# Kernel optimization log

Hardware: AMD Instinct MI355X
Metric: run time of the kernel (lower is better)

Reference implementation:

```python
import jax, jax.numpy as jnp
import numpy as np

N_NODES = 100000
N_EDGES = 1600000
IN_CH, HID_CH, LAT = 32, 32, 16


def _gcn_layer(h, W, b, src, dst, norm):
    # PyG GCNConv: h' = scatter_add(norm * (h W)[src] -> dst) + b
    h = h @ W                                   # [N, out]
    msg = h[src] * norm[:, None]                # [E+N, out] gather
    out = jax.ops.segment_sum(msg, dst, num_segments=N_NODES)
    return out + b


def setup_inputs() -> dict:
    key = jax.random.key(0)
    ks = jax.random.split(key, 8)
    x = jax.random.normal(ks[0], (N_NODES, IN_CH), dtype=jnp.float32)
    edge_index = jax.random.randint(ks[1], (2, N_EDGES), 0, N_NODES, dtype=jnp.int32)
    def glorot(k, fan_in, fan_out):
        lim = np.sqrt(6.0 / (fan_in + fan_out)).astype(np.float32)
        return jax.random.uniform(k, (fan_in, fan_out), jnp.float32, -lim, lim)
    return {
        "x": x,
        "edge_index": edge_index,
        "W1": glorot(ks[2], IN_CH, HID_CH),
        "b1": jnp.zeros((HID_CH,), jnp.float32),
        "Wmu": glorot(ks[3], HID_CH, LAT),
        "bmu": jnp.zeros((LAT,), jnp.float32),
        "Wlv": glorot(ks[4], HID_CH, LAT),
        "blv": jnp.zeros((LAT,), jnp.float32),
    }


def reference(x, edge_index, W1, b1, Wmu, bmu, Wlv, blv):
    # Add self-loops (GCNConv default add_self_loops=True)
    loops = jnp.arange(N_NODES, dtype=edge_index.dtype)
    src = jnp.concatenate([edge_index[0], loops])
    dst = jnp.concatenate([edge_index[1], loops])
    # Symmetric normalization: deg over destinations, norm = d^-1/2[src] * d^-1/2[dst]
    deg = jax.ops.segment_sum(jnp.ones_like(dst, dtype=x.dtype), dst,
                              num_segments=N_NODES)
    dinv = jnp.where(deg > 0, jax.lax.rsqrt(deg), 0.0)
    norm = dinv[src] * dinv[dst]                # [E+N]

    h = jax.nn.relu(_gcn_layer(x, W1, b1, src, dst, norm))
    mu = _gcn_layer(h, Wmu, bmu, src, dst, norm)
    logvar = _gcn_layer(h, Wlv, blv, src, dst, norm)
    return (mu, logvar)
```

## Files before the change

### kernel.cpp

```cpp
#include <hip/hip_runtime.h>
#include <hip/hip_fp16.h>

#define N_NODES 100000
#define N_EDGES 1600000
#define NCB 782
#define CAPC 2560
#define P1_BLOCKS 391
#define BKN 128
#define NBF_G 1563


__global__ __launch_bounds__(1024) void k_part1(const int* __restrict__ src,
                                                const int* __restrict__ dst,
                                                int* __restrict__ cursor1,
                                                unsigned* __restrict__ packed1) {
    __shared__ int bh[NCB];
    __shared__ int base[NCB];
    int t = threadIdx.x;
    for (int i = t; i < NCB; i += 1024) bh[i] = 0;
    __syncthreads();
    int g = blockIdx.x * 1024 + t;
    int d[4], s[4], r[4];
    if (g < N_EDGES / 4) {
        int4 d4 = reinterpret_cast<const int4*>(dst)[g];
        int4 s4 = reinterpret_cast<const int4*>(src)[g];
        d[0] = d4.x; d[1] = d4.y; d[2] = d4.z; d[3] = d4.w;
        s[0] = s4.x; s[1] = s4.y; s[2] = s4.z; s[3] = s4.w;
    } else {
        d[0] = d[1] = d[2] = d[3] = -1;
    }
#pragma unroll
    for (int j = 0; j < 4; ++j)
        if (d[j] >= 0) r[j] = atomicAdd(&bh[((unsigned)d[j]) >> 7], 1);
    __syncthreads();
    for (int i = t; i < NCB; i += 1024) {
        int c = bh[i];
        base[i] = i * CAPC + ((c > 0) ? atomicAdd(&cursor1[i], c) : 0);
    }
    __syncthreads();
#pragma unroll
    for (int j = 0; j < 4; ++j) {
        if (d[j] < 0) continue;
        unsigned dd = (unsigned)d[j];
        int b = dd >> 7;
        int pos = base[b] + r[j];
        if (pos < (b + 1) * CAPC)
            packed1[pos] = ((dd & 127u) << 17) | (unsigned)s[j];
    }
}

__global__ __launch_bounds__(512) void k_csrx(const unsigned* __restrict__ packed1,
                                              const int* __restrict__ cursor1,
                                              const float* __restrict__ x,
                                              const float* __restrict__ W1,
                                              unsigned* __restrict__ rowPack,
                                              int* __restrict__ srcSorted,
                                              __half* __restrict__ p1) {
    __shared__ int cnt[BKN];
    __shared__ int stt[BKN];
    __shared__ int wtot;
    __shared__ float sW[1024];
    int t = threadIdx.x;
    int b = blockIdx.x;
    int seg0 = b * CAPC;
    int cc = cursor1[b]; if (cc > CAPC) cc = CAPC;
    int segEnd = seg0 + cc;
    if (t < BKN) cnt[t] = 0;
    for (int i = t; i < 1024; i += 512) sW[i] = W1[i];
    unsigned pk[5]; int rk[5];
    {
        uint4 q = reinterpret_cast<const uint4*>(packed1 + seg0)[t];
        int i0 = seg0 + 4 * t;
        pk[0] = (i0     < segEnd) ? q.x : 0xFFFFFFFFu;
        pk[1] = (i0 + 1 < segEnd) ? q.y : 0xFFFFFFFFu;
        pk[2] = (i0 + 2 < segEnd) ? q.z : 0xFFFFFFFFu;
        pk[3] = (i0 + 3 < segEnd) ? q.w : 0xFFFFFFFFu;
        int i4 = seg0 + 2048 + t;
        pk[4] = (i4 < segEnd) ? packed1[i4] : 0xFFFFFFFFu;
    }
    float xv[8];
    int lane = t & 31;
    int rbase = t >> 5;
#pragma unroll
    for (int q = 0; q < 8; ++q) {
        int nd = b * BKN + rbase + q * 16;
        xv[q] = (nd < N_NODES) ? x[nd * 32 + lane] : 0.f;
    }
    __syncthreads();
#pragma unroll
    for (int j = 0; j < 5; ++j)
        if (pk[j] != 0xFFFFFFFFu) rk[j] = atomicAdd(&cnt[pk[j] >> 17], 1);
    __syncthreads();
    int v = 0, run = 0;
    if (t < BKN) {
        v = cnt[t];
        run = v;
#pragma unroll
        for (int off = 1; off < 64; off <<= 1) {
            int u = __shfl_up(run, off, 64);
            if ((t & 63) >= off) run += u;
        }
        if (t == 63) wtot = run;
    }
    __syncthreads();
    if (t < BKN) {
        if (t >= 64) run += wtot;
        int start = seg0 + run - v;
        stt[t] = start;
        int node = b * BKN + t;
        if (node < N_NODES) {
            int vc = (v < 2047) ? v : 2047;
            rowPack[node] = (unsigned)start | ((unsigned)vc << 21);
        }
    }
    __syncthreads();
#pragma unroll
    for (int j = 0; j < 5; ++j) {
        if (pk[j] == 0xFFFFFFFFu) continue;
        int pos = stt[pk[j] >> 17] + rk[j];
        srcSorted[pos] = (int)(pk[j] & 0x1FFFFu);
    }
#pragma unroll
    for (int q = 0; q < 8; ++q) {
        int r = rbase + q * 16;
        int nd = b * BKN + r;
        if (nd > N_NODES) break;
        if (nd == N_NODES) {
            p1[nd * 32 + lane] = __float2half(0.f);
            continue;
        }
        float a = 0.f;
#pragma unroll
        for (int k = 0; k < 32; ++k) {
            float xk = __shfl(xv[q], k, 32);
            a += xk * sW[k * 32 + lane];
        }
        float di = rsqrtf((float)(cnt[r] + 1));
        p1[nd * 32 + lane] = __float2half(di * a);
    }
}

__device__ __forceinline__ __half2 h2of(const float4& v, int c) {
    return reinterpret_cast<const __half2*>(&v)[c];
}

__device__ __forceinline__ void gatherRow4(const int* __restrict__ srcSorted,
                                           const float4* __restrict__ P,
                                           int beg, int end, int l,
                                           float* __restrict__ acc ) {
    for (int base = beg; base < end; base += 16) {
        int i0 = base + l,      i1 = base + 4 + l;
        int i2 = base + 8 + l,  i3 = base + 12 + l;
        int sA = (i0 < end) ? srcSorted[i0] : N_NODES;
        int sB = (i1 < end) ? srcSorted[i1] : N_NODES;
        int sC = (i2 < end) ? srcSorted[i2] : N_NODES;
        int sD = (i3 < end) ? srcSorted[i3] : N_NODES;
        float4 v0 = P[__shfl(sA, 0, 4) * 4 + l];
        float4 v1 = P[__shfl(sA, 1, 4) * 4 + l];
        float4 v2 = P[__shfl(sA, 2, 4) * 4 + l];
        float4 v3 = P[__shfl(sA, 3, 4) * 4 + l];
        float4 v4 = P[__shfl(sB, 0, 4) * 4 + l];
        float4 v5 = P[__shfl(sB, 1, 4) * 4 + l];
        float4 v6 = P[__shfl(sB, 2, 4) * 4 + l];
        float4 v7 = P[__shfl(sB, 3, 4) * 4 + l];
        float4 v8 = P[__shfl(sC, 0, 4) * 4 + l];
        float4 v9 = P[__shfl(sC, 1, 4) * 4 + l];
        float4 va = P[__shfl(sC, 2, 4) * 4 + l];
        float4 vb = P[__shfl(sC, 3, 4) * 4 + l];
        float4 vc = P[__shfl(sD, 0, 4) * 4 + l];
        float4 vd = P[__shfl(sD, 1, 4) * 4 + l];
        float4 ve = P[__shfl(sD, 2, 4) * 4 + l];
        float4 vf = P[__shfl(sD, 3, 4) * 4 + l];
#pragma unroll
        for (int c = 0; c < 4; ++c) {
            __half2 s01 = __hadd2(h2of(v0, c), h2of(v1, c));
            __half2 s23 = __hadd2(h2of(v2, c), h2of(v3, c));
            __half2 s45 = __hadd2(h2of(v4, c), h2of(v5, c));
            __half2 s67 = __hadd2(h2of(v6, c), h2of(v7, c));
            __half2 s89 = __hadd2(h2of(v8, c), h2of(v9, c));
            __half2 sab = __hadd2(h2of(va, c), h2of(vb, c));
            __half2 scd = __hadd2(h2of(vc, c), h2of(vd, c));
            __half2 sef = __hadd2(h2of(ve, c), h2of(vf, c));
            __half2 sum = __hadd2(__hadd2(__hadd2(s01, s23), __hadd2(s45, s67)),
                                  __hadd2(__hadd2(s89, sab), __hadd2(scd, sef)));
            float2 f = __half22float2(sum);
            acc[2 * c]     += f.x;
            acc[2 * c + 1] += f.y;
        }
    }
}

__global__ __launch_bounds__(256) void k_gx2(const unsigned* __restrict__ rowPack,
                                             const int* __restrict__ srcSorted,
                                             const __half* __restrict__ p1,
                                             const float* __restrict__ b1,
                                             const float* __restrict__ Wmu,
                                             const float* __restrict__ Wlv,
                                             __half* __restrict__ p2) {
    __shared__ float sW[1024];
    __shared__ float sB[32];
    int t = threadIdx.x;
    for (int i = t; i < 1024; i += 256) {
        int k = i >> 5, oc = i & 31;
        sW[i] = (oc < 16) ? Wmu[k * 16 + oc] : Wlv[k * 16 + (oc - 16)];
    }
    if (t < 32) sB[t] = b1[t];
    __syncthreads();
    int l = t & 3;
    int node = blockIdx.x * 64 + (t >> 2);
    if (node > N_NODES) return;
    const float4* P = (const float4*)p1;
    if (node == N_NODES) {
        ((float4*)p2)[node * 4 + l] = make_float4(0.f, 0.f, 0.f, 0.f);
        return;
    }
    unsigned rp = rowPack[node];
    int beg = (int)(rp & 0x1FFFFFu);
    int dg  = (int)(rp >> 21);
    float di = rsqrtf((float)(dg + 1));
    float acc[8] = {0.f, 0.f, 0.f, 0.f, 0.f, 0.f, 0.f, 0.f};
    gatherRow4(srcSorted, P, beg, beg + dg, l, acc);
    float4 ps = P[node * 4 + l];
    float h[8];
#pragma unroll
    for (int c = 0; c < 4; ++c) {
        float2 f = __half22float2(h2of(ps, c));
        h[2 * c]     = fmaxf(di * (acc[2 * c]     + f.x) + sB[8 * l + 2 * c],     0.f);
        h[2 * c + 1] = fmaxf(di * (acc[2 * c + 1] + f.y) + sB[8 * l + 2 * c + 1], 0.f);
    }
    float o[8] = {0.f, 0.f, 0.f, 0.f, 0.f, 0.f, 0.f, 0.f};
    const float4* W4 = (const float4*)sW;
#pragma unroll
    for (int m = 0; m < 4; ++m) {
#pragma unroll
        for (int j = 0; j < 8; ++j) {
            float hk = __shfl(h[j], m, 4);
            int k = 8 * m + j;
            float4 wa = W4[k * 8 + 2 * l];
            float4 wb = W4[k * 8 + 2 * l + 1];
            o[0] += hk * wa.x; o[1] += hk * wa.y; o[2] += hk * wa.z; o[3] += hk * wa.w;
            o[4] += hk * wb.x; o[5] += hk * wb.y; o[6] += hk * wb.z; o[7] += hk * wb.w;
        }
    }
    __half2 r0 = __floats2half2_rn(di * o[0], di * o[1]);
    __half2 r1 = __floats2half2_rn(di * o[2], di * o[3]);
    __half2 r2 = __floats2half2_rn(di * o[4], di * o[5]);
    __half2 r3 = __floats2half2_rn(di * o[6], di * o[7]);
    float4 st;
    st.x = *reinterpret_cast<float*>(&r0);
    st.y = *reinterpret_cast<float*>(&r1);
    st.z = *reinterpret_cast<float*>(&r2);
    st.w = *reinterpret_cast<float*>(&r3);
    ((float4*)p2)[node * 4 + l] = st;
}

__global__ __launch_bounds__(256) void k_gfin(const unsigned* __restrict__ rowPack,
                                              const int* __restrict__ srcSorted,
                                              const __half* __restrict__ p2,
                                              const float* __restrict__ bmu,
                                              const float* __restrict__ blv,
                                              float* __restrict__ out) {
    __shared__ float sB[32];
    int t = threadIdx.x;
    if (t < 32) sB[t] = (t < 16) ? bmu[t] : blv[t - 16];
    __syncthreads();
    int l = t & 3;
    int node = blockIdx.x * 64 + (t >> 2);
    if (node >= N_NODES) return;
    const float4* P = (const float4*)p2;
    unsigned rp = rowPack[node];
    int beg = (int)(rp & 0x1FFFFFu);
    int dg  = (int)(rp >> 21);
    float di = rsqrtf((float)(dg + 1));
    float acc[8] = {0.f, 0.f, 0.f, 0.f, 0.f, 0.f, 0.f, 0.f};
    gatherRow4(srcSorted, P, beg, beg + dg, l, acc);
    float4 ps = P[node * 4 + l];
    float v[8];
#pragma unroll
    for (int c = 0; c < 4; ++c) {
        float2 f = __half22float2(h2of(ps, c));
        v[2 * c]     = di * (acc[2 * c]     + f.x) + sB[8 * l + 2 * c];
        v[2 * c + 1] = di * (acc[2 * c + 1] + f.y) + sB[8 * l + 2 * c + 1];
    }
    float4 o0 = make_float4(v[0], v[1], v[2], v[3]);
    float4 o1 = make_float4(v[4], v[5], v[6], v[7]);
    float4* dst4 = (l < 2) ? (float4*)out
                           : (float4*)(out + (size_t)N_NODES * 16);
    int b4 = node * 4 + (l & 1) * 2;
    dst4[b4]     = o0;
    dst4[b4 + 1] = o1;
}

extern "C" void kernel_launch(void* const* d_in, const int* in_sizes, int n_in,
                              void* d_out, int out_size, void* d_ws, size_t ws_size,
                              hipStream_t stream) {
    const float* x   = (const float*)d_in[0];
    const int*   ei  = (const int*)d_in[1];
    const float* W1  = (const float*)d_in[2];
    const float* b1  = (const float*)d_in[3];
    const float* Wmu = (const float*)d_in[4];
    const float* bmu = (const float*)d_in[5];
    const float* Wlv = (const float*)d_in[6];
    const float* blv = (const float*)d_in[7];
    float* out = (float*)d_out;

    const int* src = ei;
    const int* dst = ei + N_EDGES;

    size_t off = 0;
    int* cursor1 = (int*)d_ws;                          off += NCB;
    unsigned* rowPack = (unsigned*)((int*)d_ws + off);  off += N_NODES;
    off = (off + 63) & ~(size_t)63;
    unsigned* packed1 = (unsigned*)((int*)d_ws + off);  off += (size_t)NCB * CAPC;
    off = (off + 63) & ~(size_t)63;
    int* srcSorted    = (int*)d_ws + off;               off += (size_t)NCB * CAPC;
    off = (off + 63) & ~(size_t)63;
    __half* p1h = (__half*)((int*)d_ws + off);          off += (size_t)(N_NODES + 1) * 16;
    off = (off + 63) & ~(size_t)63;
    __half* p2h = (__half*)((int*)d_ws + off);

    hipMemsetAsync(d_ws, 0, (size_t)NCB * sizeof(int), stream);
    k_part1<<<P1_BLOCKS, 1024, 0, stream>>>(src, dst, cursor1, packed1);
    k_csrx <<<NCB, 512, 0, stream>>>(packed1, cursor1, x, W1,
                                     rowPack, srcSorted, p1h);
    k_gx2  <<<NBF_G, 256, 0, stream>>>(rowPack, srcSorted, p1h,
                                       b1, Wmu, Wlv, p2h);
    k_gfin <<<NBF_G, 256, 0, stream>>>(rowPack, srcSorted, p2h,
                                       bmu, blv, out);
}
```

Before: 178.8 us.

## Group nodes by degree class within each bucket to balance gather work

The CSR build kernel now sorts the 128 nodes of each bucket into eight degree classes and writes a slot-indexed node id and packed row descriptor. The two gather kernels walk these slots instead of node ids, so nodes with similar degree share a wavefront and lane divergence in the edge loop drops. The padding row of p2 is zeroed in the CSR kernel, and the grid grows to cover all 782×128 slots. The cost is an extra indirection load per node and scattered, non-contiguous output writes.

Result: slower. 187.0 us (+4.6%).

```diff
diff --git a/kernel.cpp b/kernel.cpp
--- a/kernel.cpp
+++ b/kernel.cpp
@@ -7,7 +7,7 @@
 #define CAPC 2560
 #define P1_BLOCKS 391
 #define BKN 128
-#define NBF_G 1563
+#define NBF_G 1564
 
 
 __global__ __launch_bounds__(1024) void k_part1(const int* __restrict__ src,
@@ -53,12 +53,16 @@
                                               const int* __restrict__ cursor1,
                                               const float* __restrict__ x,
                                               const float* __restrict__ W1,
-                                              unsigned* __restrict__ rowPack,
+                                              int* __restrict__ nodeOf,
+                                              unsigned* __restrict__ rp2,
                                               int* __restrict__ srcSorted,
-                                              __half* __restrict__ p1) {
+                                              __half* __restrict__ p1,
+                                              __half* __restrict__ p2) {
     __shared__ int cnt[BKN];
     __shared__ int stt[BKN];
     __shared__ int wtot;
+    __shared__ int clsCnt[8];
+    __shared__ int clsOff[8];
     __shared__ float sW[1024];
     int t = threadIdx.x;
     int b = blockIdx.x;
@@ -66,7 +70,10 @@
     int cc = cursor1[b]; if (cc > CAPC) cc = CAPC;
     int segEnd = seg0 + cc;
     if (t < BKN) cnt[t] = 0;
+    if (t >= BKN && t < BKN + 8) clsCnt[t - BKN] = 0;
     for (int i = t; i < 1024; i += 512) sW[i] = W1[i];
+    if (b == 0 && t >= BKN + 8 && t < BKN + 12)
+        ((float4*)p2)[N_NODES * 4 + (t - BKN - 8)] = make_float4(0.f, 0.f, 0.f, 0.f);
     unsigned pk[5]; int rk[5];
     {
         uint4 q = reinterpret_cast<const uint4*>(packed1 + seg0)[t];
@@ -91,9 +98,11 @@
     for (int j = 0; j < 5; ++j)
         if (pk[j] != 0xFFFFFFFFu) rk[j] = atomicAdd(&cnt[pk[j] >> 17], 1);
     __syncthreads();
-    int v = 0, run = 0;
+    int v = 0, run = 0, myrank = 0, cls = 0;
     if (t < BKN) {
         v = cnt[t];
+        cls = (v + 15) >> 4; if (cls > 7) cls = 7;
+        myrank = atomicAdd(&clsCnt[cls], 1);
         run = v;
 #pragma unroll
         for (int off = 1; off < 64; off <<= 1) {
@@ -103,15 +112,14 @@
         if (t == 63) wtot = run;
     }
     __syncthreads();
+    if (t == 0) {
+        int s = 0;
+#pragma unroll
+        for (int c2 = 0; c2 < 8; ++c2) { clsOff[c2] = s; s += clsCnt[c2]; }
+    }
     if (t < BKN) {
         if (t >= 64) run += wtot;
-        int start = seg0 + run - v;
-        stt[t] = start;
-        int node = b * BKN + t;
-        if (node < N_NODES) {
-            int vc = (v < 2047) ? v : 2047;
-            rowPack[node] = (unsigned)start | ((unsigned)vc << 21);
-        }
+        stt[t] = seg0 + run - v;
     }
     __syncthreads();
 #pragma unroll
@@ -119,6 +127,13 @@
         if (pk[j] == 0xFFFFFFFFu) continue;
         int pos = stt[pk[j] >> 17] + rk[j];
         srcSorted[pos] = (int)(pk[j] & 0x1FFFFu);
+    }
+    if (t < BKN) {
+        int node = b * BKN + t;
+        int slot = b * BKN + clsOff[cls] + myrank;
+        int vc = (v < 2047) ? v : 2047;
+        nodeOf[slot] = (node < N_NODES) ? node : N_NODES;
+        rp2[slot] = (unsigned)stt[t] | ((unsigned)vc << 21);
     }
 #pragma unroll
     for (int q = 0; q < 8; ++q) {
@@ -190,7 +205,8 @@
     }
 }
 
-__global__ __launch_bounds__(256) void k_gx2(const unsigned* __restrict__ rowPack,
+__global__ __launch_bounds__(256) void k_gx2(const int* __restrict__ nodeOf,
+                                             const unsigned* __restrict__ rp2,
                                              const int* __restrict__ srcSorted,
                                              const __half* __restrict__ p1,
                                              const float* __restrict__ b1,
@@ -207,14 +223,11 @@
     if (t < 32) sB[t] = b1[t];
     __syncthreads();
     int l = t & 3;
-    int node = blockIdx.x * 64 + (t >> 2);
-    if (node > N_NODES) return;
+    int slot = blockIdx.x * 64 + (t >> 2);
+    int node = nodeOf[slot];
+    if (node >= N_NODES) return;
     const float4* P = (const float4*)p1;
-    if (node == N_NODES) {
-        ((float4*)p2)[node * 4 + l] = make_float4(0.f, 0.f, 0.f, 0.f);
-        return;
-    }
-    unsigned rp = rowPack[node];
+    unsigned rp = rp2[slot];
     int beg = (int)(rp & 0x1FFFFFu);
     int dg  = (int)(rp >> 21);
     float di = rsqrtf((float)(dg + 1));
@@ -254,7 +267,8 @@
     ((float4*)p2)[node * 4 + l] = st;
 }
 
-__global__ __launch_bounds__(256) void k_gfin(const unsigned* __restrict__ rowPack,
+__global__ __launch_bounds__(256) void k_gfin(const int* __restrict__ nodeOf,
+                                              const unsigned* __restrict__ rp2,
                                               const int* __restrict__ srcSorted,
                                               const __half* __restrict__ p2,
                                               const float* __restrict__ bmu,
@@ -265,10 +279,11 @@
     if (t < 32) sB[t] = (t < 16) ? bmu[t] : blv[t - 16];
     __syncthreads();
     int l = t & 3;
-    int node = blockIdx.x * 64 + (t >> 2);
+    int slot = blockIdx.x * 64 + (t >> 2);
+    int node = nodeOf[slot];
     if (node >= N_NODES) return;
     const float4* P = (const float4*)p2;
-    unsigned rp = rowPack[node];
+    unsigned rp = rp2[slot];
     int beg = (int)(rp & 0x1FFFFFu);
     int dg  = (int)(rp >> 21);
     float di = rsqrtf((float)(dg + 1));
@@ -309,7 +324,8 @@
 
     size_t off = 0;
     int* cursor1 = (int*)d_ws;                          off += NCB;
-    unsigned* rowPack = (unsigned*)((int*)d_ws + off);  off += N_NODES;
+    int* nodeOf  = (int*)d_ws + off;                    off += (size_t)NCB * BKN;
+    unsigned* rp2 = (unsigned*)((int*)d_ws + off);      off += (size_t)NCB * BKN;
     off = (off + 63) & ~(size_t)63;
     unsigned* packed1 = (unsigned*)((int*)d_ws + off);  off += (size_t)NCB * CAPC;
     off = (off + 63) & ~(size_t)63;
@@ -322,9 +338,9 @@
     hipMemsetAsync(d_ws, 0, (size_t)NCB * sizeof(int), stream);
     k_part1<<<P1_BLOCKS, 1024, 0, stream>>>(src, dst, cursor1, packed1);
     k_csrx <<<NCB, 512, 0, stream>>>(packed1, cursor1, x, W1,
-                                     rowPack, srcSorted, p1h);
-    k_gx2  <<<NBF_G, 256, 0, stream>>>(rowPack, srcSorted, p1h,
+                                     nodeOf, rp2, srcSorted, p1h, p2h);
+    k_gx2  <<<NBF_G, 256, 0, stream>>>(nodeOf, rp2, srcSorted, p1h,
                                        b1, Wmu, Wlv, p2h);
-    k_gfin <<<NBF_G, 256, 0, stream>>>(rowPack, srcSorted, p2h,
+    k_gfin <<<NBF_G, 256, 0, stream>>>(nodeOf, rp2, srcSorted, p2h,
                                        bmu, blv, out);
 }
```
